# Kernel tuning notes

Hardware: AMD Instinct MI355X
Metric: run time of the kernel (lower is better)

## Reference

```python
import jax, jax.numpy as jnp
import numpy as np

S, TS, K, TK = 4, 2, 8, 8
EPS = 1e-5


def setup_inputs() -> dict:
    key = jax.random.key(0)
    ks = jax.random.split(key, 20)
    n, C, t, h, w = 8, 512, 8, 32, 32
    f = jnp.float32
    d = {}
    d["x"] = jax.random.normal(ks[0], (n, C, t, h, w), f)
    d["conv1_w"] = jax.random.normal(ks[1], (K, C), f) * 0.05
    d["conv1_b"] = jax.random.normal(ks[2], (K,), f) * 0.05
    d["bn1_g"] = jax.random.uniform(ks[3], (K,), f, 0.5, 1.5)
    d["bn1_b"] = jax.random.normal(ks[4], (K,), f) * 0.05
    d["bn1_m"] = jax.random.normal(ks[5], (K,), f) * 0.05
    d["bn1_v"] = jax.random.uniform(ks[6], (K,), f, 0.5, 1.5)
    d["convp_w"] = jax.random.normal(ks[7], (S * S * K, K, S), f) * 0.05
    d["convp_b"] = jax.random.normal(ks[8], (S * S * K,), f) * 0.05
    d["convq_w"] = jax.random.normal(ks[9], (S * S * K, K, S), f) * 0.05
    d["convq_b"] = jax.random.normal(ks[10], (S * S * K,), f) * 0.05
    d["convt_w"] = jax.random.normal(ks[11], (TS * TS * TK, K, TS), f) * 0.05
    d["convt_b"] = jax.random.normal(ks[12], (TS * TS * TK,), f) * 0.05
    d["conv2_w"] = jax.random.normal(ks[13], (C, C), f) * 0.05
    d["conv2_b"] = jax.random.normal(ks[14], (C,), f) * 0.05
    d["bn2_g"] = jax.random.uniform(ks[15], (C,), f, 0.5, 1.5)
    d["bn2_b"] = jax.random.normal(ks[16], (C,), f) * 0.05
    d["bn2_m"] = jax.random.normal(ks[17], (C,), f) * 0.05
    d["bn2_v"] = jax.random.uniform(ks[18], (C,), f, 0.5, 1.5)
    return d


def _bn(x, g, b, m, v):
    # inference-mode BatchNorm3d over channel axis 1
    sh = (1, -1, 1, 1, 1)
    return (x - m.reshape(sh)) * (g / jnp.sqrt(v + EPS)).reshape(sh) + b.reshape(sh)


def reference(x, conv1_w, conv1_b, bn1_g, bn1_b, bn1_m, bn1_v,
              convp_w, convp_b, convq_w, convq_b, convt_w, convt_b,
              conv2_w, conv2_b, bn2_g, bn2_b, bn2_m, bn2_v):
    n, C, t, h, w = x.shape
    s, ts, k, tk = S, TS, K, TK
    hb, wb, tb = h // s, w // s, t // ts
    # conv1 (1x1x1) + BN + ReLU -> (n,k,t,h,w)
    o = jnp.einsum('oc,ncthw->nothw', conv1_w, x) + conv1_b.reshape(1, -1, 1, 1, 1)
    o = jax.nn.relu(_bn(o, bn1_g, bn1_b, bn1_m, bn1_v))
    # adaptive max pools: (t,s,1) and (t,1,s) -> (n,k,t,s)
    rp = o.reshape(n, k, t, s, hb, w).max(axis=(4, 5))
    cp = o.reshape(n, k, t, h, s, wb).max(axis=(3, 5))
    # conv_p / conv_q: kernel [1,s,1] / [1,1,s] collapse the s axis
    p = (jnp.einsum('oci,ncti->not', convp_w, rp) + convp_b[None, :, None]).reshape(n, k, s, s, t)
    q = (jnp.einsum('oci,ncti->not', convq_w, cp) + convq_b[None, :, None]).reshape(n, k, s, s, t)
    p = jax.nn.softmax(p, axis=3)
    q = jax.nn.softmax(q, axis=2)
    # expand across C//k channel groups, move t forward -> (n,C,t,s,s)
    g = C // k
    P = jnp.broadcast_to(p.transpose(0, 1, 4, 2, 3)[:, :, None], (n, k, g, t, s, s)).reshape(n, C, t, s, s)
    Q = jnp.broadcast_to(q.transpose(0, 1, 4, 2, 3)[:, :, None], (n, k, g, t, s, s)).reshape(n, C, t, s, s)
    # y = kron(P, I_hb) @ x @ kron(Q, I_wb)  (resize_mat is kron with identity;
    # exploit block structure instead of materializing (n,C,t,h,h) matrices)
    xr = x.reshape(n, C, t, s, hb, w)
    y = jnp.einsum('nctab,nctbuw->nctauw', P, xr).reshape(n, C, t, h, w)
    yr = y.reshape(n, C, t, h, s, wb)
    y = jnp.einsum('ncthav,nctab->ncthbv', yr, Q).reshape(n, C, t, h, w)
    # temporal mixing: adaptive avg pool to (ts,1,1), conv_t, softmax, kron(TM, I_tb)
    tp = o.reshape(n, k, ts, tb, h, w).mean(axis=(3, 4, 5))  # (n,k,ts)
    tm = jnp.einsum('oci,nci->no', convt_w, tp) + convt_b[None, :]
    tm = jax.nn.softmax(tm.reshape(n, tk, ts, ts), axis=3)
    TM = jnp.broadcast_to(tm[:, :, None], (n, tk, C // tk, ts, ts)).reshape(n, C, ts, ts)
    y = jnp.einsum('ncab,ncbuhw->ncauhw', TM, y.reshape(n, C, ts, tb, h, w)).reshape(n, C, t, h, w)
    # conv2 (1x1x1) + BN + ReLU
    y = jnp.einsum('oc,ncthw->nothw', conv2_w, y) + conv2_b.reshape(1, -1, 1, 1, 1)
    return jax.nn.relu(_bn(y, bn2_g, bn2_b, bn2_m, bn2_v))
```

## Files before the change

### kernel.cpp

```cpp
#include <hip/hip_runtime.h>
#include <math.h>

#define EPS 1e-5f

typedef __bf16 bf16x8 __attribute__((ext_vector_type(8)));
typedef float f32x4 __attribute__((ext_vector_type(4)));

__device__ static inline unsigned short f2bf(float f) {
    unsigned u = __float_as_uint(f);
    unsigned r = (u + 0x7fffu + ((u >> 16) & 1u)) >> 16;
    return (unsigned short)r;
}

__device__ static inline void load_lds16(const void* g, void* l) {
    __builtin_amdgcn_global_load_lds(
        (const __attribute__((address_space(1))) unsigned int*)g,
        (__attribute__((address_space(3))) unsigned int*)l, 16, 0, 0);
}

__global__ __launch_bounds__(256) void k_w2cast(const float* __restrict__ w2,
                                                unsigned short* __restrict__ w2bf) {
    int i = (blockIdx.x * 256 + threadIdx.x) * 4;
    float4 v = *(const float4*)&w2[i];
    ushort4 o;
    o.x = f2bf(v.x); o.y = f2bf(v.y); o.z = f2bf(v.z); o.w = f2bf(v.w);
    *(ushort4*)&w2bf[i] = o;
}

__global__ __launch_bounds__(1024) void k_conv1_pool(
    const float* __restrict__ x,  const float* __restrict__ w1,
    const float* __restrict__ b1, const float* __restrict__ g1,
    const float* __restrict__ bb1,const float* __restrict__ m1,
    const float* __restrict__ v1,
    float* __restrict__ rp, float* __restrict__ cp, float* __restrict__ tps)
{
    const int hq  = blockIdx.x;
    const int t   = blockIdx.y;
    const int nn  = blockIdx.z;
    const int tid = threadIdx.x;
    const int ch  = tid >> 8;
    const int pos = tid & 255;

    __shared__ float part[4][8][256];
    __shared__ float o_s[8 * 256];
    __shared__ float red_max[8 * 32];
    __shared__ float red_sum[8 * 32];

    const float* xb = x + (size_t)nn * 512 * 8192 + (size_t)ch * 128 * 8192
                        + t * 1024 + hq * 256 + pos;
    const float* wb = w1 + ch * 128;

    float acc[8];
#pragma unroll
    for (int k = 0; k < 8; k++) acc[k] = 0.f;

    for (int c = 0; c < 128; c += 8) {
#pragma unroll
        for (int cc = 0; cc < 8; cc++) {
            float xv = xb[(size_t)(c + cc) * 8192];
#pragma unroll
            for (int k = 0; k < 8; k++)
                acc[k] += wb[k * 512 + c + cc] * xv;
        }
    }
#pragma unroll
    for (int k = 0; k < 8; k++) part[ch][k][pos] = acc[k];
    __syncthreads();

    if (tid < 256) {
#pragma unroll
        for (int k = 0; k < 8; k++) {
            float s = part[0][k][tid] + part[1][k][tid] +
                      part[2][k][tid] + part[3][k][tid];
            float sc  = g1[k] * rsqrtf(v1[k] + EPS);
            float val = (s + b1[k] - m1[k]) * sc + bb1[k];
            o_s[k * 256 + tid] = fmaxf(val, 0.f);
        }
    }
    __syncthreads();

    if (tid < 256) {
        int k = tid >> 5, j = tid & 31;
        const float* p = &o_s[k * 256 + j * 8];
        float mx = p[0], sm = p[0];
#pragma unroll
        for (int i = 1; i < 8; i++) { mx = fmaxf(mx, p[i]); sm += p[i]; }
        red_max[k * 32 + j] = mx;
        red_sum[k * 32 + j] = sm;
    }
    __syncthreads();

    if (tid < 32) {
        int k = tid >> 2, b = tid & 3;
        float mx = red_max[k * 32 + b];
#pragma unroll
        for (int u = 1; u < 8; u++) mx = fmaxf(mx, red_max[k * 32 + u * 4 + b]);
        atomicMax((int*)&cp[((nn * 8 + k) * 8 + t) * 4 + b], __float_as_int(mx));
    }
    if (tid < 8) {
        int k = tid;
        float mx = red_max[k * 32], sm = red_sum[k * 32];
#pragma unroll
        for (int j = 1; j < 32; j++) {
            mx = fmaxf(mx, red_max[k * 32 + j]);
            sm += red_sum[k * 32 + j];
        }
        rp[((nn * 8 + k) * 8 + t) * 4 + hq] = mx;
        atomicAdd(&tps[(nn * 8 + k) * 2 + (t >> 2)], sm);
    }
}

__global__ __launch_bounds__(256) void k_pqtm(
    const float* __restrict__ rp, const float* __restrict__ cp,
    const float* __restrict__ tps,
    const float* __restrict__ pw, const float* __restrict__ pb,
    const float* __restrict__ qw, const float* __restrict__ qb,
    const float* __restrict__ tw, const float* __restrict__ tbv,
    float* __restrict__ P, float* __restrict__ Q, float* __restrict__ TM)
{
    const int nn  = blockIdx.x;
    const int tid = threadIdx.x;
    __shared__ float rps[256], cps[256], tpss[16];
    rps[tid] = rp[nn * 256 + tid];
    cps[tid] = cp[nn * 256 + tid];
    if (tid < 16) tpss[tid] = tps[nn * 16 + tid] * (1.0f / 4096.0f);
    __syncthreads();

    {
        int k = tid >> 5, a = (tid >> 3) & 3, t = tid & 7;
        float v[4];
#pragma unroll
        for (int b = 0; b < 4; b++) {
            int o = k * 16 + a * 4 + b;
            float s = pb[o];
#pragma unroll
            for (int c = 0; c < 8; c++)
#pragma unroll
                for (int i = 0; i < 4; i++)
                    s += pw[o * 32 + c * 4 + i] * rps[c * 32 + t * 4 + i];
            v[b] = s;
        }
        float mx = fmaxf(fmaxf(v[0], v[1]), fmaxf(v[2], v[3]));
        float e[4]; float sum = 0.f;
#pragma unroll
        for (int b = 0; b < 4; b++) { e[b] = expf(v[b] - mx); sum += e[b]; }
        float inv = 1.f / sum;
        int base = ((nn * 8 + k) * 8 + t) * 16 + a * 4;
#pragma unroll
        for (int b = 0; b < 4; b++) P[base + b] = e[b] * inv;
    }
    {
        int k = tid >> 5, b = (tid >> 3) & 3, t = tid & 7;
        float v[4];
#pragma unroll
        for (int a = 0; a < 4; a++) {
            int o = k * 16 + a * 4 + b;
            float s = qb[o];
#pragma unroll
            for (int c = 0; c < 8; c++)
#pragma unroll
                for (int i = 0; i < 4; i++)
                    s += qw[o * 32 + c * 4 + i] * cps[c * 32 + t * 4 + i];
            v[a] = s;
        }
        float mx = fmaxf(fmaxf(v[0], v[1]), fmaxf(v[2], v[3]));
        float e[4]; float sum = 0.f;
#pragma unroll
        for (int a = 0; a < 4; a++) { e[a] = expf(v[a] - mx); sum += e[a]; }
        float inv = 1.f / sum;
        int base = ((nn * 8 + k) * 8 + t) * 16 + b;
#pragma unroll
        for (int a = 0; a < 4; a++) Q[base + a * 4] = e[a] * inv;
    }
    if (tid < 16) {
        int kk = tid >> 1, a2 = tid & 1;
        float v[2];
#pragma unroll
        for (int b2 = 0; b2 < 2; b2++) {
            int o = kk * 4 + a2 * 2 + b2;
            float s = tbv[o];
#pragma unroll
            for (int c = 0; c < 8; c++)
#pragma unroll
                for (int i = 0; i < 2; i++)
                    s += tw[o * 16 + c * 2 + i] * tpss[c * 2 + i];
            v[b2] = s;
        }
        float mx = fmaxf(v[0], v[1]);
        float e0 = expf(v[0] - mx), e1 = expf(v[1] - mx);
        float inv = 1.f / (e0 + e1);
        TM[nn * 32 + kk * 4 + a2 * 2 + 0] = e0 * inv;
        TM[nn * 32 + kk * 4 + a2 * 2 + 1] = e1 * inv;
    }
}

__global__ __launch_bounds__(256) void k_mix(
    const float* __restrict__ x, const float* __restrict__ P,
    const float* __restrict__ Q, const float* __restrict__ TM,
    unsigned short* __restrict__ y3bf)
{
    const int u2  = blockIdx.x;
    const int c   = blockIdx.y;
    const int nn  = blockIdx.z;
    const int tid = threadIdx.x;
    const int kc  = c >> 6;

    __shared__ float x0s[1024], x1s[1024], z0s[1024], z1s[1024];

    const size_t xb = ((size_t)(nn * 512 + c) * 8 + u2) * 1024;
    *(float4*)&x0s[tid * 4] = *(const float4*)&x[xb + tid * 4];
    *(float4*)&x1s[tid * 4] = *(const float4*)&x[xb + 4096 + tid * 4];

    const float* Pb0 = &P[((nn * 8 + kc) * 8 + u2) * 16];
    const float* Pb1 = Pb0 + 4 * 16;
    const float* Qb0 = &Q[((nn * 8 + kc) * 8 + u2) * 16];
    const float* Qb1 = Qb0 + 4 * 16;
    const float* TMb = &TM[nn * 32 + kc * 4];

    const int u = tid >> 5, ww = tid & 31;
    const int bw = ww >> 3, v = ww & 7;

    float P0[4][4], P1[4][4], Q0[4], Q1[4];
#pragma unroll
    for (int a = 0; a < 4; a++) {
#pragma unroll
        for (int b = 0; b < 4; b++) {
            P0[a][b] = Pb0[a * 4 + b];
            P1[a][b] = Pb1[a * 4 + b];
        }
        Q0[a] = Qb0[a * 4 + bw];
        Q1[a] = Qb1[a * 4 + bw];
    }
    const float tm00 = TMb[0], tm01 = TMb[1], tm10 = TMb[2], tm11 = TMb[3];
    __syncthreads();

    float xv0[4], xv1[4];
#pragma unroll
    for (int bh = 0; bh < 4; bh++) {
        xv0[bh] = x0s[bh * 256 + tid];
        xv1[bh] = x1s[bh * 256 + tid];
    }
#pragma unroll
    for (int ah = 0; ah < 4; ah++) {
        float s0 = 0.f, s1 = 0.f;
#pragma unroll
        for (int bh = 0; bh < 4; bh++) {
            s0 += P0[ah][bh] * xv0[bh];
            s1 += P1[ah][bh] * xv1[bh];
        }
        z0s[ah * 256 + tid] = s0;
        z1s[ah * 256 + tid] = s1;
    }
    __syncthreads();

    const size_t ob0 = xb;
    const size_t ob1 = xb + 4096;
#pragma unroll
    for (int kidx = 0; kidx < 4; kidx++) {
        int rb = kidx * 256 + u * 32 + v;
        float y20 = 0.f, y21 = 0.f;
#pragma unroll
        for (int aw = 0; aw < 4; aw++) {
            y20 += Q0[aw] * z0s[rb + aw * 8];
            y21 += Q1[aw] * z1s[rb + aw * 8];
        }
        int p = kidx * 256 + tid;
        y3bf[ob0 + p] = f2bf(tm00 * y20 + tm01 * y21);
        y3bf[ob1 + p] = f2bf(tm10 * y20 + tm11 * y21);
    }
}

__global__ __launch_bounds__(256) void k_gemm2(
    const unsigned short* __restrict__ y3bf,
    const unsigned short* __restrict__ w2bf,
    const float* __restrict__ b2, const float* __restrict__ g2,
    const float* __restrict__ bb2,const float* __restrict__ m2,
    const float* __restrict__ v2, float* __restrict__ out)
{
    const int ct  = blockIdx.x;
    const int pt  = blockIdx.y;
    const int nn  = blockIdx.z;
    const int tid = threadIdx.x;
    const int co0 = ct * 128, p0 = pt * 128;

    __shared__ unsigned short Bs[64 * 128];
    __shared__ unsigned short As[128 * 72];
    __shared__ float sc_s[128], ba_s[128];

    if (tid < 128) {
        int co = co0 + tid;
        float sc = g2[co] * rsqrtf(v2[co] + EPS);
        sc_s[tid] = sc;
        ba_s[tid] = (b2[co] - m2[co]) * sc + bb2[co];
    }

    const int lane = tid & 63, wv = tid >> 6;
    const int wr = wv >> 1, wc = wv & 1;
    const int ln15 = lane & 15, quad = lane >> 4;

    f32x4 acc[4][4];
#pragma unroll
    for (int i = 0; i < 4; i++)
#pragma unroll
        for (int j = 0; j < 4; j++) acc[i][j] = (f32x4){0.f, 0.f, 0.f, 0.f};

    const size_t ybase = (size_t)nn * 512 * 8192 + p0;
    const int aco = tid >> 1, aseg = tid & 1;
    const unsigned short* ag = w2bf + (size_t)(co0 + aco) * 512 + aseg * 32;

    for (int c0 = 0; c0 < 512; c0 += 64) {
#pragma unroll
        for (int it = 0; it < 4; it++) {
            int rbase = wv * 16 + it * 4;
            const unsigned short* gsrc =
                y3bf + ybase + (size_t)(c0 + rbase + quad) * 8192 + ln15 * 8;
            load_lds16(gsrc, &Bs[rbase * 128]);
        }
        uint4 av4[4];
#pragma unroll
        for (int j = 0; j < 4; j++)
            av4[j] = *(const uint4*)(ag + c0 + j * 8);
#pragma unroll
        for (int j = 0; j < 4; j++)
            *(uint4*)&As[aco * 72 + aseg * 32 + j * 8] = av4[j];
        __syncthreads();

#pragma unroll
        for (int ks = 0; ks < 2; ks++) {
            bf16x8 a[4], b[4];
#pragma unroll
            for (int mi = 0; mi < 4; mi++)
                a[mi] = *(const bf16x8*)&As[(wr * 64 + mi * 16 + ln15) * 72 +
                                            ks * 32 + quad * 8];
#pragma unroll
            for (int pi = 0; pi < 4; pi++) {
                union { unsigned short u[8]; bf16x8 v; } bu;
                const unsigned short* bp =
                    &Bs[(ks * 32 + quad * 8) * 128 + wc * 64 + pi * 16 + ln15];
#pragma unroll
                for (int j = 0; j < 8; j++) bu.u[j] = bp[j * 128];
                b[pi] = bu.v;
            }
#pragma unroll
            for (int mi = 0; mi < 4; mi++)
#pragma unroll
                for (int pi = 0; pi < 4; pi++)
                    acc[mi][pi] = __builtin_amdgcn_mfma_f32_16x16x32_bf16(
                        a[mi], b[pi], acc[mi][pi], 0, 0, 0);
        }
        __syncthreads();
    }

#pragma unroll
    for (int mi = 0; mi < 4; mi++) {
        int lco = wr * 64 + mi * 16 + quad * 4;
#pragma unroll
        for (int pi = 0; pi < 4; pi++) {
            int p = p0 + wc * 64 + pi * 16 + ln15;
#pragma unroll
            for (int r = 0; r < 4; r++) {
                float vv = acc[mi][pi][r] * sc_s[lco + r] + ba_s[lco + r];
                out[((size_t)nn * 512 + co0 + lco + r) * 8192 + p] =
                    fmaxf(vv, 0.f);
            }
        }
    }
}

extern "C" void kernel_launch(void* const* d_in, const int* in_sizes, int n_in,
                              void* d_out, int out_size, void* d_ws, size_t ws_size,
                              hipStream_t stream) {
    const float* x   = (const float*)d_in[0];
    const float* w1  = (const float*)d_in[1];
    const float* b1  = (const float*)d_in[2];
    const float* g1  = (const float*)d_in[3];
    const float* bb1 = (const float*)d_in[4];
    const float* m1  = (const float*)d_in[5];
    const float* v1  = (const float*)d_in[6];
    const float* pw  = (const float*)d_in[7];
    const float* pb  = (const float*)d_in[8];
    const float* qw  = (const float*)d_in[9];
    const float* qb  = (const float*)d_in[10];
    const float* tw  = (const float*)d_in[11];
    const float* tbv = (const float*)d_in[12];
    const float* w2  = (const float*)d_in[13];
    const float* b2  = (const float*)d_in[14];
    const float* g2  = (const float*)d_in[15];
    const float* bb2 = (const float*)d_in[16];
    const float* m2  = (const float*)d_in[17];
    const float* v2  = (const float*)d_in[18];

    float* ws  = (float*)d_ws;
    float* rp  = ws;
    float* cp  = ws + 2048;
    float* tps = ws + 4096;
    float* P   = ws + 8192;
    float* Q   = ws + 16384;
    float* TM  = ws + 24576;
    unsigned short* w2bf = (unsigned short*)(ws + 32768);
    unsigned short* y3bf = (unsigned short*)(ws + 163840);

    hipMemsetAsync(ws, 0, 4224 * sizeof(float), stream);

    k_w2cast<<<dim3(256), 256, 0, stream>>>(w2, w2bf);
    k_conv1_pool<<<dim3(4, 8, 8), 1024, 0, stream>>>(x, w1, b1, g1, bb1, m1, v1,
                                                     rp, cp, tps);
    k_pqtm<<<dim3(8), 256, 0, stream>>>(rp, cp, tps, pw, pb, qw, qb, tw, tbv,
                                        P, Q, TM);
    k_mix<<<dim3(4, 512, 8), 256, 0, stream>>>(x, P, Q, TM, y3bf);
    k_gemm2<<<dim3(4, 64, 8), 256, 0, stream>>>(y3bf, w2bf, b2, g2, bb2, m2, v2,
                                                (float*)d_out);
}
```

Baseline: 409.2 us.

## Transpose mixed intermediate to channel-last and swizzle LDS in GEMM and conv1

The mixing kernel now processes 64 channels per block and writes its bf16 intermediate in position-major, channel-contiguous layout. The pointwise GEMM can then fetch both operands with direct global-to-LDS 16-byte loads into XOR-swizzled tiles, replacing strided per-element B gathers. The conv1/pool kernel is also reworked to use float4 loads per lane, 512 threads, and wave-shuffle reductions instead of multi-stage shared-memory reductions. The trade-offs are a larger shared-memory footprint per mix block, and the transposed writes depend on the swizzle indexing being correct.

```diff
diff --git a/kernel.cpp b/kernel.cpp
--- a/kernel.cpp
+++ b/kernel.cpp
@@ -27,86 +27,89 @@
     *(ushort4*)&w2bf[i] = o;
 }
 
-__global__ __launch_bounds__(1024) void k_conv1_pool(
+__global__ __launch_bounds__(512) void k_conv1_pool(
     const float* __restrict__ x,  const float* __restrict__ w1,
     const float* __restrict__ b1, const float* __restrict__ g1,
     const float* __restrict__ bb1,const float* __restrict__ m1,
     const float* __restrict__ v1,
     float* __restrict__ rp, float* __restrict__ cp, float* __restrict__ tps)
 {
-    const int hq  = blockIdx.x;
+    const int a   = blockIdx.x;
     const int t   = blockIdx.y;
     const int nn  = blockIdx.z;
     const int tid = threadIdx.x;
-    const int ch  = tid >> 8;
-    const int pos = tid & 255;
-
-    __shared__ float part[4][8][256];
-    __shared__ float o_s[8 * 256];
-    __shared__ float red_max[8 * 32];
-    __shared__ float red_sum[8 * 32];
-
-    const float* xb = x + (size_t)nn * 512 * 8192 + (size_t)ch * 128 * 8192
-                        + t * 1024 + hq * 256 + pos;
-    const float* wb = w1 + ch * 128;
-
-    float acc[8];
-#pragma unroll
-    for (int k = 0; k < 8; k++) acc[k] = 0.f;
-
-    for (int c = 0; c < 128; c += 8) {
+    const int wv  = tid >> 6;
+    const int lane= tid & 63;
+
+    __shared__ float part[8 * 8 * 256];
+
+    const int cbase = __builtin_amdgcn_readfirstlane(wv) * 64;
+    const float* xb = x + (size_t)nn * 512 * 8192 + (size_t)cbase * 8192
+                        + t * 1024 + a * 256 + lane * 4;
+    const float* wb = w1 + cbase;
+
+    f32x4 acc[8];
+#pragma unroll
+    for (int k = 0; k < 8; k++) acc[k] = (f32x4){0.f, 0.f, 0.f, 0.f};
+
+    for (int c = 0; c < 64; c += 8) {
+        float4 xv[8];
+#pragma unroll
+        for (int cc = 0; cc < 8; cc++)
+            xv[cc] = *(const float4*)(xb + (size_t)(c + cc) * 8192);
 #pragma unroll
         for (int cc = 0; cc < 8; cc++) {
-            float xv = xb[(size_t)(c + cc) * 8192];
-#pragma unroll
-            for (int k = 0; k < 8; k++)
-                acc[k] += wb[k * 512 + c + cc] * xv;
-        }
-    }
-#pragma unroll
-    for (int k = 0; k < 8; k++) part[ch][k][pos] = acc[k];
+#pragma unroll
+            for (int k = 0; k < 8; k++) {
+                float wt = wb[k * 512 + c + cc];
+                acc[k][0] += wt * xv[cc].x;
+                acc[k][1] += wt * xv[cc].y;
+                acc[k][2] += wt * xv[cc].z;
+                acc[k][3] += wt * xv[cc].w;
+            }
+        }
+    }
+#pragma unroll
+    for (int k = 0; k < 8; k++)
+        *(f32x4*)&part[(wv * 8 + k) * 256 + lane * 4] = acc[k];
     __syncthreads();
 
-    if (tid < 256) {
-#pragma unroll
-        for (int k = 0; k < 8; k++) {
-            float s = part[0][k][tid] + part[1][k][tid] +
-                      part[2][k][tid] + part[3][k][tid];
-            float sc  = g1[k] * rsqrtf(v1[k] + EPS);
-            float val = (s + b1[k] - m1[k]) * sc + bb1[k];
-            o_s[k * 256 + tid] = fmaxf(val, 0.f);
-        }
-    }
-    __syncthreads();
-
-    if (tid < 256) {
-        int k = tid >> 5, j = tid & 31;
-        const float* p = &o_s[k * 256 + j * 8];
-        float mx = p[0], sm = p[0];
-#pragma unroll
-        for (int i = 1; i < 8; i++) { mx = fmaxf(mx, p[i]); sm += p[i]; }
-        red_max[k * 32 + j] = mx;
-        red_sum[k * 32 + j] = sm;
-    }
-    __syncthreads();
-
-    if (tid < 32) {
-        int k = tid >> 2, b = tid & 3;
-        float mx = red_max[k * 32 + b];
-#pragma unroll
-        for (int u = 1; u < 8; u++) mx = fmaxf(mx, red_max[k * 32 + u * 4 + b]);
-        atomicMax((int*)&cp[((nn * 8 + k) * 8 + t) * 4 + b], __float_as_int(mx));
-    }
-    if (tid < 8) {
-        int k = tid;
-        float mx = red_max[k * 32], sm = red_sum[k * 32];
-#pragma unroll
-        for (int j = 1; j < 32; j++) {
-            mx = fmaxf(mx, red_max[k * 32 + j]);
-            sm += red_sum[k * 32 + j];
-        }
-        rp[((nn * 8 + k) * 8 + t) * 4 + hq] = mx;
-        atomicAdd(&tps[(nn * 8 + k) * 2 + (t >> 2)], sm);
+    {
+        const int k = tid >> 6;
+        f32x4 s = (f32x4){0.f, 0.f, 0.f, 0.f};
+#pragma unroll
+        for (int g = 0; g < 8; g++) {
+            f32x4 p = *(const f32x4*)&part[(g * 8 + k) * 256 + lane * 4];
+            s[0] += p[0]; s[1] += p[1]; s[2] += p[2]; s[3] += p[3];
+        }
+        const float sc = g1[k] * rsqrtf(v1[k] + EPS);
+        const float ba = (b1[k] - m1[k]) * sc + bb1[k];
+        float o0 = fmaxf(s[0] * sc + ba, 0.f);
+        float o1 = fmaxf(s[1] * sc + ba, 0.f);
+        float o2 = fmaxf(s[2] * sc + ba, 0.f);
+        float o3 = fmaxf(s[3] * sc + ba, 0.f);
+
+        float m4 = fmaxf(fmaxf(o0, o1), fmaxf(o2, o3));
+        float s4 = o0 + o1 + o2 + o3;
+
+        float mr = m4;
+#pragma unroll
+        for (int m = 32; m >= 1; m >>= 1) mr = fmaxf(mr, __shfl_xor(mr, m, 64));
+        if (lane == 0) rp[((nn * 8 + k) * 8 + t) * 4 + a] = mr;
+
+        float mc = m4;
+        mc = fmaxf(mc, __shfl_xor(mc, 1, 64));
+        mc = fmaxf(mc, __shfl_xor(mc, 8, 64));
+        mc = fmaxf(mc, __shfl_xor(mc, 16, 64));
+        mc = fmaxf(mc, __shfl_xor(mc, 32, 64));
+        if ((lane & 0x39) == 0)
+            atomicMax((int*)&cp[((nn * 8 + k) * 8 + t) * 4 + (lane >> 1)],
+                      __float_as_int(mc));
+
+        float ss = s4;
+#pragma unroll
+        for (int m = 32; m >= 1; m >>= 1) ss += __shfl_xor(ss, m, 64);
+        if (lane == 0) atomicAdd(&tps[(nn * 8 + k) * 2 + (t >> 2)], ss);
     }
 }
 
@@ -197,81 +200,93 @@
 __global__ __launch_bounds__(256) void k_mix(
     const float* __restrict__ x, const float* __restrict__ P,
     const float* __restrict__ Q, const float* __restrict__ TM,
-    unsigned short* __restrict__ y3bf)
+    unsigned short* __restrict__ y3T)
 {
-    const int u2  = blockIdx.x;
-    const int c   = blockIdx.y;
+    const int u2  = blockIdx.x >> 3;
+    const int u   = blockIdx.x & 7;
+    const int cg  = blockIdx.y;
     const int nn  = blockIdx.z;
     const int tid = threadIdx.x;
-    const int kc  = c >> 6;
-
-    __shared__ float x0s[1024], x1s[1024], z0s[1024], z1s[1024];
-
-    const size_t xb = ((size_t)(nn * 512 + c) * 8 + u2) * 1024;
-    *(float4*)&x0s[tid * 4] = *(const float4*)&x[xb + tid * 4];
-    *(float4*)&x1s[tid * 4] = *(const float4*)&x[xb + 4096 + tid * 4];
-
-    const float* Pb0 = &P[((nn * 8 + kc) * 8 + u2) * 16];
-    const float* Pb1 = Pb0 + 4 * 16;
-    const float* Qb0 = &Q[((nn * 8 + kc) * 8 + u2) * 16];
-    const float* Qb1 = Qb0 + 4 * 16;
-    const float* TMb = &TM[nn * 32 + kc * 4];
-
-    const int u = tid >> 5, ww = tid & 31;
-    const int bw = ww >> 3, v = ww & 7;
-
-    float P0[4][4], P1[4][4], Q0[4], Q1[4];
-#pragma unroll
-    for (int a = 0; a < 4; a++) {
-#pragma unroll
-        for (int b = 0; b < 4; b++) {
-            P0[a][b] = Pb0[a * 4 + b];
-            P1[a][b] = Pb1[a * 4 + b];
-        }
-        Q0[a] = Qb0[a * 4 + bw];
-        Q1[a] = Qb1[a * 4 + bw];
-    }
+
+    __shared__ float xs[16384];
+    __shared__ unsigned short ys[16384];
+
+    const size_t xbase = (size_t)nn * 512 * 8192 + (size_t)cg * 64 * 8192;
+#pragma unroll
+    for (int rr = 0; rr < 16; rr++) {
+        int id  = rr * 256 + tid;
+        int row = id >> 3;
+        int jw  = (id & 7) ^ (row & 7);
+        int tt = row >> 8, b = (row >> 6) & 3, c = row & 63;
+        const float* src = x + xbase + (size_t)c * 8192
+                             + (u2 + 4 * tt) * 1024 + (b * 8 + u) * 32 + jw * 4;
+        *(float4*)&xs[id * 4] = *(const float4*)src;
+    }
+
+    const int a = tid >> 6, c = tid & 63;
+    float Pt[2][4], Qt[2][4][4];
+#pragma unroll
+    for (int tt = 0; tt < 2; tt++) {
+        const float* Pb = &P[((nn * 8 + cg) * 8 + (u2 + 4 * tt)) * 16];
+        const float* Qb = &Q[((nn * 8 + cg) * 8 + (u2 + 4 * tt)) * 16];
+#pragma unroll
+        for (int b = 0; b < 4; b++) Pt[tt][b] = Pb[a * 4 + b];
+#pragma unroll
+        for (int aw = 0; aw < 4; aw++)
+#pragma unroll
+            for (int bw = 0; bw < 4; bw++) Qt[tt][aw][bw] = Qb[aw * 4 + bw];
+    }
+    const float* TMb = &TM[nn * 32 + cg * 4];
     const float tm00 = TMb[0], tm01 = TMb[1], tm10 = TMb[2], tm11 = TMb[3];
     __syncthreads();
 
-    float xv0[4], xv1[4];
-#pragma unroll
-    for (int bh = 0; bh < 4; bh++) {
-        xv0[bh] = x0s[bh * 256 + tid];
-        xv1[bh] = x1s[bh * 256 + tid];
-    }
-#pragma unroll
-    for (int ah = 0; ah < 4; ah++) {
+    float y1[2][32];
+#pragma unroll
+    for (int tt = 0; tt < 2; tt++) {
+#pragma unroll
+        for (int w = 0; w < 32; w++) y1[tt][w] = 0.f;
+#pragma unroll
+        for (int b = 0; b < 4; b++) {
+            int row = (tt * 4 + b) * 64 + c;
+            float pv = Pt[tt][b];
+#pragma unroll
+            for (int jw = 0; jw < 8; jw++) {
+                int chunk = row * 8 + (jw ^ (c & 7));
+                float4 xv = *(const float4*)&xs[chunk * 4];
+                y1[tt][jw * 4 + 0] += pv * xv.x;
+                y1[tt][jw * 4 + 1] += pv * xv.y;
+                y1[tt][jw * 4 + 2] += pv * xv.z;
+                y1[tt][jw * 4 + 3] += pv * xv.w;
+            }
+        }
+    }
+#pragma unroll
+    for (int w = 0; w < 32; w++) {
+        int bw = w >> 3, v = w & 7;
         float s0 = 0.f, s1 = 0.f;
 #pragma unroll
-        for (int bh = 0; bh < 4; bh++) {
-            s0 += P0[ah][bh] * xv0[bh];
-            s1 += P1[ah][bh] * xv1[bh];
-        }
-        z0s[ah * 256 + tid] = s0;
-        z1s[ah * 256 + tid] = s1;
+        for (int aw = 0; aw < 4; aw++) {
+            s0 += Qt[0][aw][bw] * y1[0][aw * 8 + v];
+            s1 += Qt[1][aw][bw] * y1[1][aw * 8 + v];
+        }
+        ys[((0 + a) * 32 + w) * 64 + c] = f2bf(tm00 * s0 + tm01 * s1);
+        ys[((4 + a) * 32 + w) * 64 + c] = f2bf(tm10 * s0 + tm11 * s1);
     }
     __syncthreads();
 
-    const size_t ob0 = xb;
-    const size_t ob1 = xb + 4096;
-#pragma unroll
-    for (int kidx = 0; kidx < 4; kidx++) {
-        int rb = kidx * 256 + u * 32 + v;
-        float y20 = 0.f, y21 = 0.f;
-#pragma unroll
-        for (int aw = 0; aw < 4; aw++) {
-            y20 += Q0[aw] * z0s[rb + aw * 8];
-            y21 += Q1[aw] * z1s[rb + aw * 8];
-        }
-        int p = kidx * 256 + tid;
-        y3bf[ob0 + p] = f2bf(tm00 * y20 + tm01 * y21);
-        y3bf[ob1 + p] = f2bf(tm10 * y20 + tm11 * y21);
+#pragma unroll
+    for (int it = 0; it < 8; it++) {
+        int id  = it * 256 + tid;
+        int row = id >> 3, jc = id & 7;
+        int tt = row >> 7, aa = (row >> 5) & 3, w = row & 31;
+        int p = (u2 + 4 * tt) * 1024 + (aa * 8 + u) * 32 + w;
+        uint4 val = *(const uint4*)&ys[id * 8];
+        *(uint4*)&y3T[((size_t)nn * 8192 + p) * 512 + cg * 64 + jc * 8] = val;
     }
 }
 
 __global__ __launch_bounds__(256) void k_gemm2(
-    const unsigned short* __restrict__ y3bf,
+    const unsigned short* __restrict__ y3T,
     const unsigned short* __restrict__ w2bf,
     const float* __restrict__ b2, const float* __restrict__ g2,
     const float* __restrict__ bb2,const float* __restrict__ m2,
@@ -283,8 +298,8 @@
     const int tid = threadIdx.x;
     const int co0 = ct * 128, p0 = pt * 128;
 
-    __shared__ unsigned short Bs[64 * 128];
-    __shared__ unsigned short As[128 * 72];
+    __shared__ unsigned short As[8192];
+    __shared__ unsigned short Bs[8192];
     __shared__ float sc_s[128], ba_s[128];
 
     if (tid < 128) {
@@ -298,48 +313,43 @@
     const int wr = wv >> 1, wc = wv & 1;
     const int ln15 = lane & 15, quad = lane >> 4;
 
+    const int lrow = lane >> 3;
+    const int jc   = (lane & 7) ^ lrow;
+
     f32x4 acc[4][4];
 #pragma unroll
     for (int i = 0; i < 4; i++)
 #pragma unroll
         for (int j = 0; j < 4; j++) acc[i][j] = (f32x4){0.f, 0.f, 0.f, 0.f};
 
-    const size_t ybase = (size_t)nn * 512 * 8192 + p0;
-    const int aco = tid >> 1, aseg = tid & 1;
-    const unsigned short* ag = w2bf + (size_t)(co0 + aco) * 512 + aseg * 32;
+    const unsigned short* Ag = w2bf + (size_t)co0 * 512;
+    const unsigned short* Bg = y3T + ((size_t)nn * 8192 + p0) * 512;
 
     for (int c0 = 0; c0 < 512; c0 += 64) {
 #pragma unroll
         for (int it = 0; it < 4; it++) {
-            int rbase = wv * 16 + it * 4;
-            const unsigned short* gsrc =
-                y3bf + ybase + (size_t)(c0 + rbase + quad) * 8192 + ln15 * 8;
-            load_lds16(gsrc, &Bs[rbase * 128]);
-        }
-        uint4 av4[4];
-#pragma unroll
-        for (int j = 0; j < 4; j++)
-            av4[j] = *(const uint4*)(ag + c0 + j * 8);
-#pragma unroll
-        for (int j = 0; j < 4; j++)
-            *(uint4*)&As[aco * 72 + aseg * 32 + j * 8] = av4[j];
+            int rb = (wv * 4 + it) * 8;
+            load_lds16(Ag + (size_t)(rb + lrow) * 512 + c0 + jc * 8,
+                       &As[(wv * 4 + it) * 512]);
+            load_lds16(Bg + (size_t)(rb + lrow) * 512 + c0 + jc * 8,
+                       &Bs[(wv * 4 + it) * 512]);
+        }
         __syncthreads();
 
 #pragma unroll
         for (int ks = 0; ks < 2; ks++) {
             bf16x8 a[4], b[4];
 #pragma unroll
-            for (int mi = 0; mi < 4; mi++)
-                a[mi] = *(const bf16x8*)&As[(wr * 64 + mi * 16 + ln15) * 72 +
-                                            ks * 32 + quad * 8];
+            for (int mi = 0; mi < 4; mi++) {
+                int row = wr * 64 + mi * 16 + ln15;
+                int chunk = row * 8 + ((ks * 4 + quad) ^ (row & 7));
+                a[mi] = *(const bf16x8*)&As[chunk * 8];
+            }
 #pragma unroll
             for (int pi = 0; pi < 4; pi++) {
-                union { unsigned short u[8]; bf16x8 v; } bu;
-                const unsigned short* bp =
-                    &Bs[(ks * 32 + quad * 8) * 128 + wc * 64 + pi * 16 + ln15];
-#pragma unroll
-                for (int j = 0; j < 8; j++) bu.u[j] = bp[j * 128];
-                b[pi] = bu.v;
+                int row = wc * 64 + pi * 16 + ln15;
+                int chunk = row * 8 + ((ks * 4 + quad) ^ (row & 7));
+                b[pi] = *(const bf16x8*)&Bs[chunk * 8];
             }
 #pragma unroll
             for (int mi = 0; mi < 4; mi++)
@@ -398,16 +408,16 @@
     float* Q   = ws + 16384;
     float* TM  = ws + 24576;
     unsigned short* w2bf = (unsigned short*)(ws + 32768);
-    unsigned short* y3bf = (unsigned short*)(ws + 163840);
+    unsigned short* y3T  = (unsigned short*)(ws + 163840);
 
     hipMemsetAsync(ws, 0, 4224 * sizeof(float), stream);
 
     k_w2cast<<<dim3(256), 256, 0, stream>>>(w2, w2bf);
-    k_conv1_pool<<<dim3(4, 8, 8), 1024, 0, stream>>>(x, w1, b1, g1, bb1, m1, v1,
-                                                     rp, cp, tps);
+    k_conv1_pool<<<dim3(4, 8, 8), 512, 0, stream>>>(x, w1, b1, g1, bb1, m1, v1,
+                                                    rp, cp, tps);
     k_pqtm<<<dim3(8), 256, 0, stream>>>(rp, cp, tps, pw, pb, qw, qb, tw, tbv,
                                         P, Q, TM);
-    k_mix<<<dim3(4, 512, 8), 256, 0, stream>>>(x, P, Q, TM, y3bf);
-    k_gemm2<<<dim3(4, 64, 8), 256, 0, stream>>>(y3bf, w2bf, b2, g2, bb2, m2, v2,
+    k_mix<<<dim3(32, 8, 8), 256, 0, stream>>>(x, P, Q, TM, y3T);
+    k_gemm2<<<dim3(4, 64, 8), 256, 0, stream>>>(y3T, w2bf, b2, g2, bb2, m2, v2,
                                                 (float*)d_out);
 }
```

Result: faster. 365.6 us (-10.7%).
